# Kernel optimization log

Measured on AMD Instinct MI355X. Metric: run time of the kernel, lower is better.

The kernel has to match this reference:

```python
import jax, jax.numpy as jnp
import numpy as np

NUM_TYPES = 200
TOK_DIM = 10000
SMALL_DIM = 64
IN_DIM = 32 + 32 + SMALL_DIM  # 128
NUM_EDGE_TYPES = 3
STEPS = 4
BLOCKS = 2
PROJ_DIM = 128
N_NODES = 100000
N_EDGES = 600000
N_GRAPHS = 64


def setup_inputs() -> dict:
    key = jax.random.key(0)
    ks = jax.random.split(key, 20)
    s = 0.05
    inp = {
        'x_type': jax.random.randint(ks[0], (N_NODES,), 0, NUM_TYPES),
        'x_tok': jax.random.randint(ks[1], (N_NODES,), 0, TOK_DIM + 1),
        'x_small': jax.random.normal(ks[2], (N_NODES, SMALL_DIM), jnp.float32),
        'edge_index': jax.random.randint(ks[3], (2, N_EDGES), 0, N_NODES),
        'edge_type': jax.random.randint(ks[4], (N_EDGES,), 0, NUM_EDGE_TYPES),
        'batch': jnp.sort(jax.random.randint(ks[5], (N_NODES,), 0, N_GRAPHS)),
        # learned params
        'type_emb': jax.random.normal(ks[6], (NUM_TYPES, 32), jnp.float32),
        'tok_emb': jax.random.normal(ks[7], (TOK_DIM + 1, 32), jnp.float32),
        'msg_W': jax.random.normal(ks[8], (NUM_EDGE_TYPES, IN_DIM, IN_DIM), jnp.float32) * s,
        'msg_b': jax.random.normal(ks[9], (NUM_EDGE_TYPES, IN_DIM), jnp.float32) * s,
        'W_ih': jax.random.normal(ks[10], (3 * IN_DIM, IN_DIM), jnp.float32) * s,
        'W_hh': jax.random.normal(ks[11], (3 * IN_DIM, IN_DIM), jnp.float32) * s,
        'b_ih': jax.random.normal(ks[12], (3 * IN_DIM,), jnp.float32) * s,
        'b_hh': jax.random.normal(ks[13], (3 * IN_DIM,), jnp.float32) * s,
        'proj_W1': jax.random.normal(ks[14], (PROJ_DIM, IN_DIM), jnp.float32) * s,
        'proj_b1': jax.random.normal(ks[15], (PROJ_DIM,), jnp.float32) * s,
        'proj_W2': jax.random.normal(ks[16], (1, PROJ_DIM), jnp.float32) * s,
        'proj_b2': jax.random.normal(ks[17], (1,), jnp.float32) * s,
    }
    return inp


def _gru_cell(m, h, W_ih, W_hh, b_ih, b_hh):
    # torch.nn.GRU single step
    gi = m @ W_ih.T + b_ih  # [N, 3H]
    gh = h @ W_hh.T + b_hh
    i_r, i_z, i_n = jnp.split(gi, 3, axis=-1)
    h_r, h_z, h_n = jnp.split(gh, 3, axis=-1)
    r = jax.nn.sigmoid(i_r + h_r)
    z = jax.nn.sigmoid(i_z + h_z)
    n = jnp.tanh(i_n + r * h_n)
    return (1.0 - z) * n + z * h


def reference(x_type, x_tok, x_small, edge_index, edge_type, batch,
              type_emb, tok_emb, msg_W, msg_b,
              W_ih, W_hh, b_ih, b_hh,
              proj_W1, proj_b1, proj_W2, proj_b2):
    n = x_type.shape[0]
    x = jnp.concatenate([type_emb[x_type], tok_emb[x_tok], x_small], axis=-1)  # [N, IN_DIM]
    src, dst = edge_index[0], edge_index[1]
    for _ in range(BLOCKS * STEPS):
        # transform every node once per edge type: [T, N, D]
        h_all = jnp.einsum('ni,toi->tno', x, msg_W) + msg_b[:, None, :]
        # per-edge message = typed linear of source node (gather)
        m = h_all[edge_type, src]  # [E, D]
        agg = jax.ops.segment_sum(m, dst, num_segments=n)  # summed over edge types too
        x = _gru_cell(agg, x, W_ih, W_hh, b_ih, b_hh)
    # global mean pool over graphs
    sums = jax.ops.segment_sum(x, batch, num_segments=N_GRAPHS)
    counts = jax.ops.segment_sum(jnp.ones((n,), x.dtype), batch, num_segments=N_GRAPHS)
    pooled = sums / jnp.maximum(counts, 1.0)[:, None]
    h = jax.nn.relu(pooled @ proj_W1.T + proj_b1)  # dropout = identity in eval
    logits = (h @ proj_W2.T + proj_b2).reshape(-1)
    return logits
```

## Files before the change

### kernel.cpp

```cpp
#include <hip/hip_runtime.h>
#include <stdint.h>


typedef _Float16 f16;
typedef _Float16 v8hf __attribute__((ext_vector_type(8)));
typedef _Float16 v2hf __attribute__((ext_vector_type(2)));
typedef float    v16f __attribute__((ext_vector_type(16)));

#define S1F 49152
#define S2F 49152
#define GHF 49152

__device__ __forceinline__ float sigf(float a){
  return __fdividef(1.0f, 1.0f + __expf(-a));
}
__device__ __forceinline__ float tanhf_fast(float a){
  return 1.0f - __fdividef(2.0f, __expf(2.0f*a) + 1.0f);
}

__global__ void k_diag(float* out, int n, float v){
  int i = threadIdx.x; if(i<n) out[i] = v;
}

__global__ void k_embed(const int* __restrict__ xtype, const int* __restrict__ xtok,
                        const float* __restrict__ xsmall,
                        const float* __restrict__ temb, const float* __restrict__ kemb,
                        f16* __restrict__ xb, int N){
  int n = blockIdx.x; int j = threadIdx.x;
  if(n>=N) return;
  float v;
  if(j<32)       v = temb[xtype[n]*32 + j];
  else if(j<64)  v = kemb[xtok[n]*32 + (j-32)];
  else           v = xsmall[(size_t)n*64 + (j-64)];
  xb[(size_t)n*128 + j] = (f16)v;
}

__global__ void k_wprep2(const float* __restrict__ msg_W,
                         const float* __restrict__ W_ih,
                         const float* __restrict__ W_hh,
                         f16* __restrict__ WpF){
  int i = blockIdx.x*256 + threadIdx.x;
  if(i >= S1F + S2F + GHF) return;
  int seg = i / 49152;
  int i2 = i % 49152;
  int grp = i2/512, rem = i2%512;
  int lane = rem/8, j = rem%8;
  float w;
  if(seg == 0){
    int tile = grp/24, ks = grp%24;
    int n = tile*32 + (lane&31);
    int k = ks*16 + (lane>>5)*8 + j;
    w = msg_W[(k>>7)*16384 + n*128 + (k&127)];
  } else {
    int tile = grp/8, ks = grp%8;
    int n = tile*32 + (lane&31);
    int k = ks*16 + (lane>>5)*8 + j;
    const float* W = (seg==1)? W_ih : W_hh;
    w = W[n*128 + k];
  }
  WpF[i] = (f16)w;
}

__global__ void k_hist3(const int* __restrict__ dst, const int* __restrict__ et,
                        int* __restrict__ deg3, int E){
  int e = blockIdx.x*blockDim.x + threadIdx.x;
  if(e<E) atomicAdd(&deg3[dst[e]*3 + et[e]], 1);
}

__global__ void k_scan1(const int* __restrict__ deg, int n, int* __restrict__ part, int* __restrict__ bsum){
  __shared__ int s[256];
  int t = threadIdx.x;
  int base = blockIdx.x*1024 + t*4;
  int v[4]; int sum=0;
  #pragma unroll
  for(int k=0;k<4;k++){ int i=base+k; int d=(i<n)?deg[i]:0; sum+=d; v[k]=sum; }
  s[t]=sum; __syncthreads();
  for(int off=1;off<256;off<<=1){
    int add = (t>=off)? s[t-off] : 0;
    __syncthreads();
    s[t]+=add;
    __syncthreads();
  }
  int excl = (t>0)? s[t-1] : 0;
  #pragma unroll
  for(int k=0;k<4;k++){ int i=base+k; if(i<n) part[i]=v[k]+excl; }
  if(t==255) bsum[blockIdx.x] = s[255];
}

__global__ void k_scan2(const int* __restrict__ bsum, int nb, int* __restrict__ carry){
  if(threadIdx.x==0 && blockIdx.x==0){
    int c=0;
    for(int b=0;b<nb;b++){ carry[b]=c; c+=bsum[b]; }
  }
}

__global__ void k_finalize(const int* __restrict__ part, const int* __restrict__ deg,
                           const int* __restrict__ carry, int n,
                           int* __restrict__ rowptr, int* __restrict__ cursor){
  int i = blockIdx.x*blockDim.x + threadIdx.x;
  if(i>=n) return;
  int incl = part[i] + carry[i>>10];
  rowptr[i+1] = incl;
  cursor[i] = incl - deg[i];
  if(i==0) rowptr[0]=0;
}

__global__ void k_fill3(const int* __restrict__ src, const int* __restrict__ dst,
                        const int* __restrict__ et, int* __restrict__ cursor,
                        int* __restrict__ pay, int E){
  int e = blockIdx.x*blockDim.x + threadIdx.x;
  if(e>=E) return;
  int pos = atomicAdd(&cursor[dst[e]*3 + et[e]], 1);
  pay[pos] = src[e] << 8;
}

__global__ void k_gather3_f(const f16* __restrict__ xb, const int* __restrict__ rp3,
                            const int* __restrict__ pay, f16* __restrict__ s, int N){
  int tid = threadIdx.x;
  int lane = tid & 63;
  int h = lane >> 4;
  int c8b = (lane & 15)*16;
  const char* xbb = (const char*)xb;
  int n = blockIdx.x*16 + (tid>>6)*4 + h;
  bool valid = (n < N);
  int nn = valid ? n : (N-1);
  int b = nn*3;
  int lo = rp3[b], e0 = rp3[b+1], e1 = rp3[b+2], hi = rp3[b+3];
  if(!valid){ lo = 0; e0 = 0; e1 = 0; hi = 0; }
  v8hf a0 = {}, a1 = {}, a2 = {};
  int len = hi - lo;
  int t1 = lo + len/3;
  int t2 = lo + (2*len)/3;
  int iA = lo, iB = t1, iC = t2;
  while(iA < t1 && iB < t2 && iC < hi){
    int pA = pay[iA], pB = pay[iB], pC = pay[iC];
    v8hf uA = *(const v8hf*)(xbb + pA + c8b);
    v8hf uB = *(const v8hf*)(xbb + pB + c8b);
    v8hf uC = *(const v8hf*)(xbb + pC + c8b);
    if(iA < e0)      a0 += uA;
    else if(iA < e1) a1 += uA;
    else             a2 += uA;
    if(iB < e0)      a0 += uB;
    else if(iB < e1) a1 += uB;
    else             a2 += uB;
    if(iC < e0)      a0 += uC;
    else if(iC < e1) a1 += uC;
    else             a2 += uC;
    iA++; iB++; iC++;
  }
  for(; iA < t1; iA++){
    v8hf u = *(const v8hf*)(xbb + pay[iA] + c8b);
    if(iA < e0)      a0 += u;
    else if(iA < e1) a1 += u;
    else             a2 += u;
  }
  for(; iB < t2; iB++){
    v8hf u = *(const v8hf*)(xbb + pay[iB] + c8b);
    if(iB < e0)      a0 += u;
    else if(iB < e1) a1 += u;
    else             a2 += u;
  }
  for(; iC < hi; iC++){
    v8hf u = *(const v8hf*)(xbb + pay[iC] + c8b);
    if(iC < e0)      a0 += u;
    else if(iC < e1) a1 += u;
    else             a2 += u;
  }
  if(valid){
    char* sb = (char*)s + (size_t)n*768 + c8b;
    *(v8hf*)(sb)       = a0;
    *(v8hf*)(sb + 256) = a1;
    *(v8hf*)(sb + 512) = a2;
  }
}

#define SSTR 392
#define XSTR 136
__global__ __launch_bounds__(256,3) void k_mega2s(
    const f16* __restrict__ xb_old, f16* __restrict__ xb_new,
    const f16* __restrict__ s, const f16* __restrict__ WpF,
    const int* __restrict__ deg3, const float* __restrict__ msg_b,
    const float* __restrict__ b_ih, const float* __restrict__ b_hh, int M)
{
  __shared__ f16 Ss[32*SSTR];
  __shared__ f16 Ax[32*XSTR];
  __shared__ float Dg[96];
  int tid = threadIdx.x, lane = tid & 63, w = tid >> 6;
  int lrow = lane & 31, q = lane >> 5;
  int row0 = blockIdx.x * 32;

  #pragma unroll
  for(int p=0;p<2;p++){
    int ch = tid + p*256;
    int row = ch>>4, c8 = (ch&15)*8;
    int gr = row0 + row; if(gr >= M) gr = M-1;
    *(v8hf*)&Ax[row*XSTR + c8] = *(const v8hf*)(xb_old + (size_t)gr*128 + c8);
  }
  #pragma unroll
  for(int p=0;p<6;p++){
    int ch = tid + p*256;
    int row = ch/48, c8 = (ch%48)*8;
    int gr = row0 + row; if(gr >= M) gr = M-1;
    *(v8hf*)&Ss[row*SSTR + c8] = *(const v8hf*)(s + (size_t)gr*384 + c8);
  }
  if(tid < 96){
    int node = row0 + tid/3;
    Dg[tid] = (node < M) ? (float)deg3[node*3 + (tid - (tid/3)*3)] : 0.f;
  }
  __syncthreads();

  int jf = w*32 + lrow;
  int rq4 = 4*q;

  v16f accy = {};
  #pragma unroll
  for(int ks=0; ks<24; ks++){
    int kb = ks*16 + q*8;
    v8hf a0 = *(const v8hf*)&Ss[lrow*SSTR + kb];
    v8hf by = *(const v8hf*)(WpF + (size_t)(w*24 + ks)*512 + lane*8);
    accy = __builtin_amdgcn_mfma_f32_32x32x16_f16(a0, by, accy, 0,0,0);
  }
  {
    float m0 = msg_b[jf], m1 = msg_b[128+jf], m2 = msg_b[256+jf];
    #pragma unroll
    for(int r=0;r<16;r++){
      int gl = (r&3) + 8*(r>>2) + rq4;
      accy[r] += Dg[gl*3]*m0 + Dg[gl*3+1]*m1 + Dg[gl*3+2]*m2;
    }
  }
  __syncthreads();
  f16* Ay = Ss;
  #pragma unroll
  for(int r=0;r<16;r++){
    int gl = (r&3) + 8*(r>>2) + rq4;
    Ay[gl*XSTR + jf] = (f16)accy[r];
  }
  __syncthreads();

  v16f acc0 = {}, acc1 = {}, acc2 = {};
  #pragma unroll
  for(int ks=0; ks<8; ks++){
    int kb = ks*16 + q*8;
    v8hf a0 = *(const v8hf*)&Ay[lrow*XSTR + kb];
    v8hf b0 = *(const v8hf*)(WpF + S1F + (size_t)((0*4+w)*8 + ks)*512 + lane*8);
    v8hf b1 = *(const v8hf*)(WpF + S1F + (size_t)((1*4+w)*8 + ks)*512 + lane*8);
    v8hf b2 = *(const v8hf*)(WpF + S1F + (size_t)((2*4+w)*8 + ks)*512 + lane*8);
    acc0 = __builtin_amdgcn_mfma_f32_32x32x16_f16(a0, b0, acc0, 0,0,0);
    acc1 = __builtin_amdgcn_mfma_f32_32x32x16_f16(a0, b1, acc1, 0,0,0);
    acc2 = __builtin_amdgcn_mfma_f32_32x32x16_f16(a0, b2, acc2, 0,0,0);
  }
  v2hf gp2[8];
  #pragma unroll
  for(int rp=0; rp<8; rp++){
    v2hf t; t[0] = (f16)acc2[2*rp]; t[1] = (f16)acc2[2*rp+1];
    gp2[rp] = t;
  }

  v16f accn = {};
  #pragma unroll
  for(int ks=0; ks<8; ks++){
    int kb = ks*16 + q*8;
    v8hf a0 = *(const v8hf*)&Ax[lrow*XSTR + kb];
    v8hf b0 = *(const v8hf*)(WpF + S1F + S2F + (size_t)((0*4+w)*8 + ks)*512 + lane*8);
    v8hf b1 = *(const v8hf*)(WpF + S1F + S2F + (size_t)((1*4+w)*8 + ks)*512 + lane*8);
    v8hf b2 = *(const v8hf*)(WpF + S1F + S2F + (size_t)((2*4+w)*8 + ks)*512 + lane*8);
    acc0 = __builtin_amdgcn_mfma_f32_32x32x16_f16(a0, b0, acc0, 0,0,0);
    acc1 = __builtin_amdgcn_mfma_f32_32x32x16_f16(a0, b1, acc1, 0,0,0);
    accn = __builtin_amdgcn_mfma_f32_32x32x16_f16(a0, b2, accn, 0,0,0);
  }

  __syncthreads();

  float br = b_ih[jf]     + b_hh[jf];
  float bz = b_ih[128+jf] + b_hh[128+jf];
  float bi2 = b_ih[256+jf], bh2 = b_hh[256+jf];
  #pragma unroll
  for(int r=0;r<16;r++){
    int gl = (r&3) + 8*(r>>2) + rq4;
    float rg = sigf(acc0[r] + br);
    float zg = sigf(acc1[r] + bz);
    float in_ = (float)gp2[r>>1][r&1] + bi2;
    float hn  = accn[r] + bh2;
    float nn = tanhf_fast(in_ + rg*hn);
    float xo = (float)Ax[gl*XSTR + jf];
    Ax[gl*XSTR + jf] = (f16)((1.f - zg)*nn + zg*xo);
  }
  __syncthreads();
  #pragma unroll
  for(int p=0;p<2;p++){
    int ch = tid + p*256;
    int row = ch>>4, c8 = (ch&15)*8;
    int gr = row0 + row;
    if(gr < M)
      *(v8hf*)(xb_new + (size_t)gr*128 + c8) = *(const v8hf*)&Ax[row*XSTR + c8];
  }
}

__device__ __forceinline__ int lb_batch(const int* __restrict__ batch, int N, int g){
  int lo=0, hi=N;
  while(lo<hi){ int mid=(lo+hi)>>1; if(batch[mid]<g) lo=mid+1; else hi=mid; }
  return lo;
}

__global__ void k_pool2(const f16* __restrict__ xb, const int* __restrict__ batch,
                        float* __restrict__ pooled, int N){
  int g = blockIdx.x, slice = blockIdx.y;
  int j = threadIdx.x;
  int lo = lb_batch(batch,N,g), hi = lb_batch(batch,N,g+1);
  float acc = 0.f;
  for(int r=lo+slice; r<hi; r+=32) acc += (float)xb[(size_t)r*128 + j];
  atomicAdd(&pooled[g*128+j], acc);
}

__global__ void k_head(const float* __restrict__ pooled, const int* __restrict__ batch, int N,
                       const float* __restrict__ W1, const float* __restrict__ b1,
                       const float* __restrict__ W2, const float* __restrict__ b2,
                       float* __restrict__ out){
  int g = blockIdx.x; int j = threadIdx.x;
  __shared__ float p[128];
  __shared__ float red[128];
  int lo = lb_batch(batch,N,g), hi = lb_batch(batch,N,g+1);
  float c = (float)(hi-lo); if(c < 1.f) c = 1.f;
  p[j] = pooled[g*128+j] / c;
  __syncthreads();
  float acc = b1[j];
  #pragma unroll 4
  for(int i=0;i<128;i++) acc += W1[j*128+i]*p[i];
  float v = (acc>0.f?acc:0.f) * W2[j];
  red[j] = v; __syncthreads();
  for(int s=64;s>0;s>>=1){ if(j<s) red[j]+=red[j+s]; __syncthreads(); }
  if(j==0) out[g] = red[0] + b2[0];
}

extern "C" void kernel_launch(void* const* d_in, const int* in_sizes, int n_in,
                              void* d_out, int out_size, void* d_ws, size_t ws_size,
                              hipStream_t stream){
  const int*   x_type    = (const int*)d_in[0];
  const int*   x_tok     = (const int*)d_in[1];
  const float* x_small   = (const float*)d_in[2];
  const int*   edge_index= (const int*)d_in[3];
  const int*   edge_type = (const int*)d_in[4];
  const int*   batch     = (const int*)d_in[5];
  const float* type_emb  = (const float*)d_in[6];
  const float* tok_emb   = (const float*)d_in[7];
  const float* msg_W     = (const float*)d_in[8];
  const float* msg_b     = (const float*)d_in[9];
  const float* W_ih      = (const float*)d_in[10];
  const float* W_hh      = (const float*)d_in[11];
  const float* b_ih      = (const float*)d_in[12];
  const float* b_hh      = (const float*)d_in[13];
  const float* pW1       = (const float*)d_in[14];
  const float* pb1       = (const float*)d_in[15];
  const float* pW2       = (const float*)d_in[16];
  const float* pb2       = (const float*)d_in[17];
  float* out = (float*)d_out;

  int N = in_sizes[0];
  int E = in_sizes[3]/2;
  const int* src = edge_index;
  const int* dst = edge_index + E;
  int n3 = 3*N;
  int nch = (n3+1023)/1024;

  char* w = (char*)d_ws;
  size_t off = 0;
  auto alloc = [&](size_t bytes)->char*{ char* p = w + off; off += (bytes + 511) & ~511ull; return p; };
  f16*   xb0    = (f16*)alloc((size_t)N*128*2);
  f16*   xb1    = (f16*)alloc((size_t)N*128*2);
  f16*   s      = (f16*)alloc((size_t)N*384*2);
  int*   deg3   = (int*)alloc((size_t)n3*4);
  int*   part   = (int*)alloc((size_t)n3*4);
  int*   rp3    = (int*)alloc((size_t)(n3+1)*4);
  int*   cursor = (int*)alloc((size_t)n3*4);
  int*   pay    = (int*)alloc((size_t)E*4);
  int*   bsum   = (int*)alloc((size_t)nch*4);
  int*   carry  = (int*)alloc((size_t)nch*4);
  f16*   WpF    = (f16*)alloc((size_t)(S1F+S2F+GHF)*2);
  float* pooled = (float*)alloc(64*128*4);
  if(off > ws_size){
    k_diag<<<1,64,0,stream>>>(out, out_size, 1.0e6f + (float)(ws_size>>20));
    return;
  }

  const int tb = 256;
  hipMemsetAsync(deg3, 0, (size_t)n3*4, stream);
  k_wprep2  <<<(S1F+S2F+GHF+255)/256, 256, 0, stream>>>(msg_W, W_ih, W_hh, WpF);
  k_hist3   <<<(E+tb-1)/tb, tb, 0, stream>>>(dst, edge_type, deg3, E);
  k_scan1   <<<nch, 256, 0, stream>>>(deg3, n3, part, bsum);
  k_scan2   <<<1, 64, 0, stream>>>(bsum, nch, carry);
  k_finalize<<<(n3+tb-1)/tb, tb, 0, stream>>>(part, deg3, carry, n3, rp3, cursor);
  k_fill3   <<<(E+tb-1)/tb, tb, 0, stream>>>(src, dst, edge_type, cursor, pay, E);
  k_embed   <<<N, 128, 0, stream>>>(x_type, x_tok, x_small, type_emb, tok_emb, xb0, N);

  int nblk = (N+31)/32;
  f16* xin = xb0;
  f16* xout = xb1;
  for(int it=0; it<8; it++){
    k_gather3_f<<<(N+15)/16, 256, 0, stream>>>(xin, rp3, pay, s, N);
    k_mega2s   <<<nblk, 256, 0, stream>>>(xin, xout, s, WpF, deg3, msg_b, b_ih, b_hh, N);
    f16* tmp = xin; xin = xout; xout = tmp;
  }
  hipMemsetAsync(pooled, 0, 64*128*4, stream);
  k_pool2<<<dim3(64,32), 128, 0, stream>>>(xin, batch, pooled, N);
  k_head <<<64, 128, 0, stream>>>(pooled, batch, N, pW1, pb1, pW2, pb2, out);
}
```

Before: 1.041 ms.

## Store gathered aggregates pre-swizzled and load them into LDS via global_load_lds

The gather kernel now writes the per-node aggregate buffer in 32-row blocks with an XOR swizzle on 16-byte columns. The fused GRU kernel copies each block straight into shared memory with global_load_lds, skipping the register round-trip and padded stride, and reads MFMA operands through the matching swizzle to avoid bank conflicts. The buffer is padded to whole blocks, so tail rows are read as uninitialized padding instead of being clamped. The direct LDS loads rely on a wave-uniform destination layout, and their ordering is only enforced by the existing barrier.

```diff
diff --git a/kernel.cpp b/kernel.cpp
--- a/kernel.cpp
+++ b/kernel.cpp
@@ -167,14 +167,14 @@
     else             a2 += u;
   }
   if(valid){
-    char* sb = (char*)s + (size_t)n*768 + c8b;
-    *(v8hf*)(sb)       = a0;
-    *(v8hf*)(sb + 256) = a1;
-    *(v8hf*)(sb + 512) = a2;
-  }
-}
-
-#define SSTR 392
+    char* sb = (char*)s + (size_t)(n>>5)*24576 + (size_t)(n&31)*768;
+    int x = (n&7)<<4;
+    *(v8hf*)(sb + (c8b ^ x))       = a0;
+    *(v8hf*)(sb + 256 + (c8b ^ x)) = a1;
+    *(v8hf*)(sb + 512 + (c8b ^ x)) = a2;
+  }
+}
+
 #define XSTR 136
 __global__ __launch_bounds__(256,3) void k_mega2s(
     const f16* __restrict__ xb_old, f16* __restrict__ xb_new,
@@ -182,13 +182,25 @@
     const int* __restrict__ deg3, const float* __restrict__ msg_b,
     const float* __restrict__ b_ih, const float* __restrict__ b_hh, int M)
 {
-  __shared__ f16 Ss[32*SSTR];
-  __shared__ f16 Ax[32*XSTR];
+  __shared__ __align__(16) f16 Ss[12288];
+  __shared__ __align__(16) f16 Ax[32*XSTR];
   __shared__ float Dg[96];
   int tid = threadIdx.x, lane = tid & 63, w = tid >> 6;
   int lrow = lane & 31, q = lane >> 5;
   int row0 = blockIdx.x * 32;
 
+  {
+    const char* sblk = (const char*)s + (size_t)blockIdx.x*24576;
+    #pragma unroll
+    for(int p=0;p<6;p++){
+      int chb = w*64 + p*256;
+      const char* gsrc = sblk + (size_t)(chb + lane)*16;
+      char* ldst = (char*)Ss + (size_t)chb*16;
+      __builtin_amdgcn_global_load_lds(
+          (const __attribute__((address_space(1))) uint32_t*)gsrc,
+          (__attribute__((address_space(3))) uint32_t*)ldst, 16, 0, 0);
+    }
+  }
   #pragma unroll
   for(int p=0;p<2;p++){
     int ch = tid + p*256;
@@ -196,13 +208,6 @@
     int gr = row0 + row; if(gr >= M) gr = M-1;
     *(v8hf*)&Ax[row*XSTR + c8] = *(const v8hf*)(xb_old + (size_t)gr*128 + c8);
   }
-  #pragma unroll
-  for(int p=0;p<6;p++){
-    int ch = tid + p*256;
-    int row = ch/48, c8 = (ch%48)*8;
-    int gr = row0 + row; if(gr >= M) gr = M-1;
-    *(v8hf*)&Ss[row*SSTR + c8] = *(const v8hf*)(s + (size_t)gr*384 + c8);
-  }
   if(tid < 96){
     int node = row0 + tid/3;
     Dg[tid] = (node < M) ? (float)deg3[node*3 + (tid - (tid/3)*3)] : 0.f;
@@ -211,12 +216,13 @@
 
   int jf = w*32 + lrow;
   int rq4 = 4*q;
+  int swz = (lrow&7)<<4;
 
   v16f accy = {};
   #pragma unroll
   for(int ks=0; ks<24; ks++){
-    int kb = ks*16 + q*8;
-    v8hf a0 = *(const v8hf*)&Ss[lrow*SSTR + kb];
+    int bytecol = (ks*32 + q*16) ^ swz;
+    v8hf a0 = *(const v8hf*)((const char*)Ss + lrow*768 + bytecol);
     v8hf by = *(const v8hf*)(WpF + (size_t)(w*24 + ks)*512 + lane*8);
     accy = __builtin_amdgcn_mfma_f32_32x32x16_f16(a0, by, accy, 0,0,0);
   }
@@ -361,13 +367,14 @@
   const int* dst = edge_index + E;
   int n3 = 3*N;
   int nch = (n3+1023)/1024;
+  int nblk = (N+31)/32;
 
   char* w = (char*)d_ws;
   size_t off = 0;
   auto alloc = [&](size_t bytes)->char*{ char* p = w + off; off += (bytes + 511) & ~511ull; return p; };
   f16*   xb0    = (f16*)alloc((size_t)N*128*2);
   f16*   xb1    = (f16*)alloc((size_t)N*128*2);
-  f16*   s      = (f16*)alloc((size_t)N*384*2);
+  f16*   s      = (f16*)alloc((size_t)nblk*24576);
   int*   deg3   = (int*)alloc((size_t)n3*4);
   int*   part   = (int*)alloc((size_t)n3*4);
   int*   rp3    = (int*)alloc((size_t)(n3+1)*4);
@@ -392,7 +399,6 @@
   k_fill3   <<<(E+tb-1)/tb, tb, 0, stream>>>(src, dst, edge_type, cursor, pay, E);
   k_embed   <<<N, 128, 0, stream>>>(x_type, x_tok, x_small, type_emb, tok_emb, xb0, N);
 
-  int nblk = (N+31)/32;
   f16* xin = xb0;
   f16* xout = xb1;
   for(int it=0; it<8; it++){
```

Result: slower. 1.080 ms (+3.7%).

## Sort nodes by in-degree for gather load balance and vectorize embedding

Applied to the files above, without the earlier changes.

Adds a counting sort of nodes by total in-degree (histogram, scan, scatter into an order array). The gather kernel then processes nodes in that order, so the four nodes sharing a wavefront have similar edge counts and less divergence. The embedding kernel becomes a grid-stride loop writing 8 halves per thread. The cost is a few extra setup kernels and an indirection through order, which makes the reads of rp3 and the writes of s for each node non-sequential.

```diff
diff --git a/kernel.cpp b/kernel.cpp
--- a/kernel.cpp
+++ b/kernel.cpp
@@ -10,6 +10,7 @@
 #define S1F 49152
 #define S2F 49152
 #define GHF 49152
+#define NBIN 1024
 
 __device__ __forceinline__ float sigf(float a){
   return __fdividef(1.0f, 1.0f + __expf(-a));
@@ -22,17 +23,22 @@
   int i = threadIdx.x; if(i<n) out[i] = v;
 }
 
-__global__ void k_embed(const int* __restrict__ xtype, const int* __restrict__ xtok,
-                        const float* __restrict__ xsmall,
-                        const float* __restrict__ temb, const float* __restrict__ kemb,
-                        f16* __restrict__ xb, int N){
-  int n = blockIdx.x; int j = threadIdx.x;
-  if(n>=N) return;
-  float v;
-  if(j<32)       v = temb[xtype[n]*32 + j];
-  else if(j<64)  v = kemb[xtok[n]*32 + (j-32)];
-  else           v = xsmall[(size_t)n*64 + (j-64)];
-  xb[(size_t)n*128 + j] = (f16)v;
+__global__ void k_embed2(const int* __restrict__ xtype, const int* __restrict__ xtok,
+                         const float* __restrict__ xsmall,
+                         const float* __restrict__ temb, const float* __restrict__ kemb,
+                         f16* __restrict__ xb, int N){
+  int total = N*16;
+  for(int c = blockIdx.x*blockDim.x + threadIdx.x; c < total; c += gridDim.x*blockDim.x){
+    int n = c >> 4, j8 = (c & 15)*8;
+    const float* src;
+    if(j8 < 32)      src = temb + (size_t)xtype[n]*32 + j8;
+    else if(j8 < 64) src = kemb + (size_t)xtok[n]*32 + (j8-32);
+    else             src = xsmall + (size_t)n*64 + (j8-64);
+    v8hf t;
+    #pragma unroll
+    for(int k=0;k<8;k++) t[k] = (f16)src[k];
+    *(v8hf*)&xb[(size_t)n*128 + j8] = t;
+  }
 }
 
 __global__ void k_wprep2(const float* __restrict__ msg_W,
@@ -114,17 +120,37 @@
   pay[pos] = src[e] << 8;
 }
 
-__global__ void k_gather3_f(const f16* __restrict__ xb, const int* __restrict__ rp3,
-                            const int* __restrict__ pay, f16* __restrict__ s, int N){
+__global__ void k_deghist(const int* __restrict__ rp3, int* __restrict__ dhist, int N){
+  int n = blockIdx.x*blockDim.x + threadIdx.x;
+  if(n < N){
+    int d = rp3[3*n+3] - rp3[3*n];
+    if(d > NBIN-1) d = NBIN-1;
+    atomicAdd(&dhist[d], 1);
+  }
+}
+__global__ void k_degscatter(const int* __restrict__ rp3, int* __restrict__ dcur,
+                             int* __restrict__ order, int N){
+  int n = blockIdx.x*blockDim.x + threadIdx.x;
+  if(n < N){
+    int d = rp3[3*n+3] - rp3[3*n];
+    if(d > NBIN-1) d = NBIN-1;
+    int pos = atomicAdd(&dcur[d], 1);
+    order[pos] = n;
+  }
+}
+
+__global__ void k_gather3_g(const f16* __restrict__ xb, const int* __restrict__ rp3,
+                            const int* __restrict__ pay, const int* __restrict__ order,
+                            f16* __restrict__ s, int N){
   int tid = threadIdx.x;
   int lane = tid & 63;
   int h = lane >> 4;
   int c8b = (lane & 15)*16;
   const char* xbb = (const char*)xb;
-  int n = blockIdx.x*16 + (tid>>6)*4 + h;
-  bool valid = (n < N);
-  int nn = valid ? n : (N-1);
-  int b = nn*3;
+  int oi = blockIdx.x*16 + (tid>>6)*4 + h;
+  bool valid = (oi < N);
+  int n = valid ? order[oi] : 0;
+  int b = n*3;
   int lo = rp3[b], e0 = rp3[b+1], e1 = rp3[b+2], hi = rp3[b+3];
   if(!valid){ lo = 0; e0 = 0; e1 = 0; hi = 0; }
   v8hf a0 = {}, a1 = {}, a2 = {};
@@ -361,6 +387,7 @@
   const int* dst = edge_index + E;
   int n3 = 3*N;
   int nch = (n3+1023)/1024;
+  int nblk = (N+31)/32;
 
   char* w = (char*)d_ws;
   size_t off = 0;
@@ -375,6 +402,13 @@
   int*   pay    = (int*)alloc((size_t)E*4);
   int*   bsum   = (int*)alloc((size_t)nch*4);
   int*   carry  = (int*)alloc((size_t)nch*4);
+  int*   order  = (int*)alloc((size_t)N*4);
+  int*   dhist  = (int*)alloc((size_t)NBIN*4);
+  int*   dpart  = (int*)alloc((size_t)NBIN*4);
+  int*   dcur   = (int*)alloc((size_t)NBIN*4);
+  int*   drp    = (int*)alloc((size_t)(NBIN+1)*4);
+  int*   dbsum  = (int*)alloc(64*4);
+  int*   dcarry = (int*)alloc(64*4);
   f16*   WpF    = (f16*)alloc((size_t)(S1F+S2F+GHF)*2);
   float* pooled = (float*)alloc(64*128*4);
   if(off > ws_size){
@@ -384,19 +418,24 @@
 
   const int tb = 256;
   hipMemsetAsync(deg3, 0, (size_t)n3*4, stream);
+  hipMemsetAsync(dhist, 0, (size_t)NBIN*4, stream);
   k_wprep2  <<<(S1F+S2F+GHF+255)/256, 256, 0, stream>>>(msg_W, W_ih, W_hh, WpF);
   k_hist3   <<<(E+tb-1)/tb, tb, 0, stream>>>(dst, edge_type, deg3, E);
   k_scan1   <<<nch, 256, 0, stream>>>(deg3, n3, part, bsum);
   k_scan2   <<<1, 64, 0, stream>>>(bsum, nch, carry);
   k_finalize<<<(n3+tb-1)/tb, tb, 0, stream>>>(part, deg3, carry, n3, rp3, cursor);
   k_fill3   <<<(E+tb-1)/tb, tb, 0, stream>>>(src, dst, edge_type, cursor, pay, E);
-  k_embed   <<<N, 128, 0, stream>>>(x_type, x_tok, x_small, type_emb, tok_emb, xb0, N);
-
-  int nblk = (N+31)/32;
+  k_deghist <<<(N+tb-1)/tb, tb, 0, stream>>>(rp3, dhist, N);
+  k_scan1   <<<1, 256, 0, stream>>>(dhist, NBIN, dpart, dbsum);
+  k_scan2   <<<1, 64, 0, stream>>>(dbsum, 1, dcarry);
+  k_finalize<<<(NBIN+tb-1)/tb, tb, 0, stream>>>(dpart, dhist, dcarry, NBIN, drp, dcur);
+  k_degscatter<<<(N+tb-1)/tb, tb, 0, stream>>>(rp3, dcur, order, N);
+  k_embed2  <<<2048, 256, 0, stream>>>(x_type, x_tok, x_small, type_emb, tok_emb, xb0, N);
+
   f16* xin = xb0;
   f16* xout = xb1;
   for(int it=0; it<8; it++){
-    k_gather3_f<<<(N+15)/16, 256, 0, stream>>>(xin, rp3, pay, s, N);
+    k_gather3_g<<<(N+15)/16, 256, 0, stream>>>(xin, rp3, pay, order, s, N);
     k_mega2s   <<<nblk, 256, 0, stream>>>(xin, xout, s, WpF, deg3, msg_b, b_ih, b_hh, N);
     f16* tmp = xin; xin = xout; xout = tmp;
   }
```

After: 1.788 ms. +71.7%, slower.
